# Kernel optimization log

Measured on AMD Instinct MI355X. Metric: run time of the kernel, lower is better.

Reference implementation:

```python
import jax, jax.numpy as jnp
import numpy as np

DIM = 64      # fixed by fuse=BasicConv2d(64,64)
HEADS = 8
B, H, W = 16, 128, 128
CPH = DIM // HEADS  # 8 channels per head


def conv2d(x, w, groups=1, pad=1):
    # x: [B,C,H,W], w: [O, C//groups, kh, kw]
    return jax.lax.conv_general_dilated(
        x, w, window_strides=(1, 1), padding=[(pad, pad), (pad, pad)],
        dimension_numbers=("NCHW", "OIHW", "NCHW"), feature_group_count=groups)


def setup_inputs() -> dict:
    key = jax.random.key(0)
    ks = jax.random.split(key, 8)
    y = jax.random.normal(ks[0], (B, DIM, H, W), jnp.float32)
    # conv3d kernels collapse to their middle depth slice (depth-1 input, zero pad)
    w_qkv = jax.random.normal(ks[1], (3 * DIM, DIM), jnp.float32) * 0.05        # 1x1x1 qkv
    w_dw = jax.random.normal(ks[2], (3 * DIM, 1, 3, 3), jnp.float32) * 0.1      # depthwise 3x3
    w_proj = jax.random.normal(ks[3], (DIM, DIM), jnp.float32) * 0.05           # 1x1x1 project_out
    w_fc = jax.random.normal(ks[4], (9, 3 * HEADS), jnp.float32) * 0.1          # fc: 24->9
    b_fc = jnp.zeros((9,), jnp.float32)
    w_dep = jax.random.normal(ks[5], (DIM, 9, 3, 3), jnp.float32) * 0.1         # grouped: 72->64, groups=8
    b_dep = jnp.zeros((DIM,), jnp.float32)
    temperature = jnp.ones((HEADS, 1, 1), jnp.float32)
    w_fuse = jax.random.normal(ks[6], (DIM, DIM, 3, 3), jnp.float32) * 0.05     # fuse conv, no bias
    bn_gamma = jnp.ones((DIM,), jnp.float32)
    bn_beta = jnp.zeros((DIM,), jnp.float32)
    bn_mean = jnp.zeros((DIM,), jnp.float32)
    bn_var = jnp.ones((DIM,), jnp.float32)
    return dict(y=y, w_qkv=w_qkv, w_dw=w_dw, w_proj=w_proj, w_fc=w_fc, b_fc=b_fc,
                w_dep=w_dep, b_dep=b_dep, temperature=temperature, w_fuse=w_fuse,
                bn_gamma=bn_gamma, bn_beta=bn_beta, bn_mean=bn_mean, bn_var=bn_var)


def reference(y, w_qkv, w_dw, w_proj, w_fc, b_fc, w_dep, b_dep, temperature,
              w_fuse, bn_gamma, bn_beta, bn_mean, bn_var):
    b, c, h, w = y.shape
    # qkv 1x1 conv then 3x3 depthwise conv (groups = 3*DIM)
    qkv = jnp.einsum('oc,bchw->bohw', w_qkv, y)                 # [b,192,h,w]
    qkv = conv2d(qkv, w_dw, groups=3 * DIM, pad=1)
    # dynamic kernel generation branch: flat reshape (row-major, matches torch)
    f_all = qkv.reshape(b, h * w, 3 * HEADS, CPH).transpose(0, 2, 1, 3)  # [b,24,hw,8]
    f_all = jnp.einsum('oc,bcne->bone', w_fc, f_all) + b_fc[None, :, None, None]  # [b,9,hw,8]
    f_conv = f_all.transpose(0, 3, 1, 2).reshape(b, 9 * CPH, h, w)       # [b,72,h,w]
    out_conv = conv2d(f_conv, w_dep, groups=CPH, pad=1) + b_dep[None, :, None, None]
    # channel (transposed) attention with L2-normalize + temperature + softmax
    q, k, v = jnp.split(qkv, 3, axis=1)
    def to_heads(t):
        return t.reshape(b, HEADS, CPH, h * w)
    q, k, v = to_heads(q), to_heads(k), to_heads(v)
    q = q / jnp.maximum(jnp.linalg.norm(q, axis=-1, keepdims=True), 1e-12)
    k = k / jnp.maximum(jnp.linalg.norm(k, axis=-1, keepdims=True), 1e-12)
    attn = jnp.einsum('bhcn,bhdn->bhcd', q, k) * temperature[None]       # [b,8,8,8]
    attn = jax.nn.softmax(attn, axis=-1)
    out = jnp.einsum('bhcd,bhdn->bhcn', attn, v).reshape(b, DIM, h, w)
    out = jnp.einsum('oc,bchw->bohw', w_proj, out)
    output = out + out_conv
    # fuse: conv3x3 (no bias) + BatchNorm (inference stats), then residual + ReLU
    fused = conv2d(output, w_fuse, pad=1)
    scale = (bn_gamma / jnp.sqrt(bn_var + 1e-5))[None, :, None, None]
    fused = (fused - bn_mean[None, :, None, None]) * scale + bn_beta[None, :, None, None]
    return jax.nn.relu(fused + y)
```

## Files before the change

### kernel.cpp

```cpp
#include <hip/hip_runtime.h>
#include <hip/hip_bf16.h>

#define BN 16
#define CC 64
#define HH 128
#define WW 128
#define HW 16384
#define C3 192
#define NHEADS 8


__global__ __launch_bounds__(256) void k_qkv1(const float* __restrict__ y,
                                              const float* __restrict__ w_qkv,
                                              float* __restrict__ out, int chunk) {
    __shared__ float ws[64 * 64];
    int tid = threadIdx.x;
    for (int i = tid; i < 4096; i += 256) {
        int c = i >> 6, o = i & 63;
        ws[i] = w_qkv[(chunk * 64 + o) * 64 + c];
    }
    __syncthreads();
    int bid = blockIdx.x;
    int b = bid >> 6;
    int ptile = bid & 63;
    int pxg = tid & 127;
    int osub = tid >> 7;
    int p0 = ptile * 256 + pxg * 2;
    const float* yb = y + (size_t)b * CC * HW + p0;
    float acc0[32];
    float acc1[32];
#pragma unroll
    for (int o = 0; o < 32; ++o) { acc0[o] = 0.f; acc1[o] = 0.f; }
    for (int c = 0; c < 64; ++c) {
        float2 yv = *(const float2*)(yb + (size_t)c * HW);
        const float* wr = &ws[c * 64 + osub * 32];
#pragma unroll
        for (int o = 0; o < 32; ++o) {
            float w = wr[o];
            acc0[o] = fmaf(w, yv.x, acc0[o]);
            acc1[o] = fmaf(w, yv.y, acc1[o]);
        }
    }
    float* ob = out + (size_t)b * 64 * HW + (size_t)(osub * 32) * HW + p0;
#pragma unroll
    for (int o = 0; o < 32; ++o) {
        *(float2*)(ob + (size_t)o * HW) = make_float2(acc0[o], acc1[o]);
    }
}

__global__ __launch_bounds__(256) void k_dw(const float* __restrict__ in,
                                            const float* __restrict__ w_dw,
                                            float* __restrict__ out, int chunk) {
    int bid = blockIdx.x;
    int tid = threadIdx.x;
    int b = bid >> 11;
    int rem = bid & 2047;
    int ch = rem >> 5;
    int tile = rem & 31;
    int pp = tile * 512 + tid * 2;
    int py = pp >> 7, px = pp & 127;
    const float* ib = in + ((size_t)b * 64 + ch) * HW;
    const float* wr = w_dw + (chunk * 64 + ch) * 9;
    float w[9];
#pragma unroll
    for (int i = 0; i < 9; ++i) w[i] = wr[i];
    float a0 = 0.f, a1 = 0.f;
#pragma unroll
    for (int ky = 0; ky < 3; ++ky) {
        int yy = py + ky - 1;
        bool yok = (unsigned)yy < 128u;
#pragma unroll
        for (int kx = 0; kx < 4; ++kx) {
            int xx = px + kx - 1;
            bool ok = yok && ((unsigned)xx < 128u);
            float v = ok ? ib[yy * 128 + xx] : 0.f;
            if (kx < 3) a0 = fmaf(w[ky * 3 + kx], v, a0);
            if (kx > 0) a1 = fmaf(w[ky * 3 + kx - 1], v, a1);
        }
    }
    *(float2*)(out + ((size_t)b * C3 + chunk * 64 + ch) * HW + pp) = make_float2(a0, a1);
}

__global__ __launch_bounds__(256) void k_fc(const float* __restrict__ qkv,
                                            const float* __restrict__ w_fc,
                                            const float* __restrict__ b_fc,
                                            float* __restrict__ fconv) {
    __shared__ float wf[216];
    __shared__ float bf[9];
    __shared__ float sx[32 * 193];
    int tid = threadIdx.x;
    if (tid < 216) wf[tid] = w_fc[tid];
    if (tid < 9) bf[tid] = b_fc[tid];
    int bid = blockIdx.x;
    int b = bid >> 9;
    int n0 = (bid & 511) * 32;
    const float* src = qkv + (size_t)b * C3 * HW + (size_t)n0 * 192;
    for (int f4 = tid; f4 < 1536; f4 += 256) {
        int f = f4 * 4;
        int nl = f / 192;
        int r = f - nl * 192;
        float4 v = *(const float4*)(src + f);
        float* d = &sx[nl * 193 + r];
        d[0] = v.x; d[1] = v.y; d[2] = v.z; d[3] = v.w;
    }
    __syncthreads();
    int e = tid >> 5, n = tid & 31;
    const float* xr = &sx[n * 193 + e];
    float acc[9];
#pragma unroll
    for (int o = 0; o < 9; ++o) acc[o] = bf[o];
#pragma unroll
    for (int g = 0; g < 24; ++g) {
        float xv = xr[g * 8];
#pragma unroll
        for (int o = 0; o < 9; ++o) acc[o] = fmaf(wf[o * 24 + g], xv, acc[o]);
    }
    float* ob = fconv + (size_t)b * 72 * HW + n0 + n;
#pragma unroll
    for (int o = 0; o < 9; ++o) ob[(size_t)(e * 9 + o) * HW] = acc[o];
}

#define GST 20
__global__ __launch_bounds__(256) void k_gconv(const float* __restrict__ fconv,
                                               const float* __restrict__ w_dep,
                                               const float* __restrict__ b_dep,
                                               float* __restrict__ outO) {
    __shared__ __align__(16) float sm_in[9 * 18 * GST];
    __shared__ __align__(16) float sm_w[81 * 8];
    __shared__ float sm_b[8];
    int tid = threadIdx.x;
    int bid = blockIdx.x;
    int b = bid >> 9;
    int rem = bid & 511;
    int grp = rem >> 6;
    int tile = rem & 63;
    int ty0 = (tile >> 3) * 16, tx0 = (tile & 7) * 16;
    const float* ibase = fconv + ((size_t)b * 72 + grp * 9) * HW;
    for (int i = tid; i < 9 * 324; i += 256) {
        int c = i / 324;
        int r2 = i - c * 324;
        int r = r2 / 18;
        int q = r2 - r * 18;
        int yy = ty0 + r - 1, xx = tx0 + q - 1;
        sm_in[c * (18 * GST) + r * GST + q] =
            ((unsigned)yy < 128u && (unsigned)xx < 128u)
                ? ibase[(size_t)c * HW + yy * 128 + xx] : 0.f;
    }
    for (int i = tid; i < 648; i += 256) {
        int o = i & 7;
        int ik = i >> 3;
        sm_w[i] = w_dep[(size_t)(grp * 8 + o) * 81 + ik];
    }
    if (tid < 8) sm_b[tid] = b_dep[grp * 8 + tid];
    __syncthreads();
    int row = tid >> 4, col = tid & 15;
    float acc[8];
#pragma unroll
    for (int o = 0; o < 8; ++o) acc[o] = sm_b[o];
#pragma unroll
    for (int ic = 0; ic < 9; ++ic) {
        float nb[3][3];
        const float* sc = &sm_in[ic * (18 * GST) + row * GST + col];
#pragma unroll
        for (int r = 0; r < 3; ++r)
#pragma unroll
            for (int q = 0; q < 3; ++q) nb[r][q] = sc[r * GST + q];
        const float* wp = &sm_w[ic * 72];
#pragma unroll
        for (int k = 0; k < 9; ++k) {
            float4 w0 = *(const float4*)(wp + k * 8);
            float4 w1 = *(const float4*)(wp + k * 8 + 4);
            float v = nb[k / 3][k % 3];
            acc[0] = fmaf(w0.x, v, acc[0]);
            acc[1] = fmaf(w0.y, v, acc[1]);
            acc[2] = fmaf(w0.z, v, acc[2]);
            acc[3] = fmaf(w0.w, v, acc[3]);
            acc[4] = fmaf(w1.x, v, acc[4]);
            acc[5] = fmaf(w1.y, v, acc[5]);
            acc[6] = fmaf(w1.z, v, acc[6]);
            acc[7] = fmaf(w1.w, v, acc[7]);
        }
    }
    float* ob = outO + ((size_t)b * 64 + grp * 8) * HW + (ty0 + row) * 128 + tx0 + col;
#pragma unroll
    for (int o = 0; o < 8; ++o) ob[(size_t)o * HW] = acc[o];
}

__global__ __launch_bounds__(256) void k_attn_p(const float* __restrict__ qkv,
                                                float* __restrict__ partial) {
    __shared__ float red[4][64];
    __shared__ float redq[4][8];
    __shared__ float redk[4][8];
    int bid = blockIdx.x;
    int b = bid >> 5, h = (bid >> 2) & 7, seg = bid & 3;
    int tid = threadIdx.x;
    const float* Q = qkv + ((size_t)b * C3 + h * 8) * HW;
    const float* K = Q + (size_t)64 * HW;
    float acc[64], qs[8], ks[8];
#pragma unroll
    for (int j = 0; j < 64; ++j) acc[j] = 0.f;
#pragma unroll
    for (int d = 0; d < 8; ++d) { qs[d] = 0.f; ks[d] = 0.f; }
    int iend = (seg + 1) * 4096;
    for (int i = seg * 4096 + tid; i < iend; i += 256) {
        float qv[8], kv[8];
#pragma unroll
        for (int d = 0; d < 8; ++d) {
            qv[d] = Q[(size_t)d * HW + i];
            kv[d] = K[(size_t)d * HW + i];
        }
#pragma unroll
        for (int d = 0; d < 8; ++d) {
            qs[d] = fmaf(qv[d], qv[d], qs[d]);
            ks[d] = fmaf(kv[d], kv[d], ks[d]);
        }
#pragma unroll
        for (int c = 0; c < 8; ++c)
#pragma unroll
            for (int d = 0; d < 8; ++d)
                acc[c * 8 + d] = fmaf(qv[c], kv[d], acc[c * 8 + d]);
    }
#pragma unroll
    for (int j = 0; j < 64; ++j) {
#pragma unroll
        for (int off = 32; off; off >>= 1) acc[j] += __shfl_down(acc[j], off, 64);
    }
#pragma unroll
    for (int d = 0; d < 8; ++d) {
#pragma unroll
        for (int off = 32; off; off >>= 1) {
            qs[d] += __shfl_down(qs[d], off, 64);
            ks[d] += __shfl_down(ks[d], off, 64);
        }
    }
    int lane = tid & 63, wv = tid >> 6;
    if (lane == 0) {
#pragma unroll
        for (int j = 0; j < 64; ++j) red[wv][j] = acc[j];
#pragma unroll
        for (int d = 0; d < 8; ++d) { redq[wv][d] = qs[d]; redk[wv][d] = ks[d]; }
    }
    __syncthreads();
    float* outp = partial + (size_t)bid * 80;
    if (tid < 64) {
        outp[tid] = red[0][tid] + red[1][tid] + red[2][tid] + red[3][tid];
    } else if (tid < 72) {
        int d = tid - 64;
        outp[64 + d] = redq[0][d] + redq[1][d] + redq[2][d] + redq[3][d];
    } else if (tid < 80) {
        int d = tid - 72;
        outp[72 + d] = redk[0][d] + redk[1][d] + redk[2][d] + redk[3][d];
    }
}

__global__ __launch_bounds__(256) void k_attn_f(const float* __restrict__ partial,
                                                const float* __restrict__ temperature,
                                                float* __restrict__ attn) {
    __shared__ float sm[80];
    __shared__ float lg[64];
    int bh = blockIdx.x;
    int h = bh & 7;
    int tid = threadIdx.x;
    if (tid < 80) {
        const float* pp = partial + (size_t)bh * 4 * 80 + tid;
        sm[tid] = pp[0] + pp[80] + pp[160] + pp[240];
    }
    __syncthreads();
    if (tid < 64) {
        int c = tid >> 3, d = tid & 7;
        float invq = 1.f / fmaxf(sqrtf(sm[64 + c]), 1e-12f);
        float invk = 1.f / fmaxf(sqrtf(sm[72 + d]), 1e-12f);
        lg[tid] = sm[tid] * invq * invk * temperature[h];
    }
    __syncthreads();
    if (tid < 8) {
        int c = tid;
        float m = lg[c * 8];
#pragma unroll
        for (int d = 1; d < 8; ++d) m = fmaxf(m, lg[c * 8 + d]);
        float ssum = 0.f, ex[8];
#pragma unroll
        for (int d = 0; d < 8; ++d) { ex[d] = expf(lg[c * 8 + d] - m); ssum += ex[d]; }
        float inv = 1.f / ssum;
#pragma unroll
        for (int d = 0; d < 8; ++d)
            attn[(size_t)bh * 64 + c * 8 + d] = ex[d] * inv;
    }
}

__global__ __launch_bounds__(256) void k_av_proj(const float* __restrict__ qkv,
                                                 const float* __restrict__ attn,
                                                 const float* __restrict__ w_proj,
                                                 float* __restrict__ outO) {
    __shared__ float at[512];
    __shared__ float wp[4096];
    int tid = threadIdx.x;
    int bid = blockIdx.x;
    int b = bid >> 6, tile = bid & 63;
    for (int i = tid; i < 512; i += 256) at[i] = attn[b * 512 + i];
    for (int i = tid; i < 4096; i += 256) {
        int c = i >> 6, o = i & 63;
        wp[i] = w_proj[o * 64 + c];
    }
    __syncthreads();
    int p = tile * 256 + tid;
    const float* vb = qkv + ((size_t)b * C3 + 128) * HW + p;
    float av[64];
#pragma unroll
    for (int h = 0; h < 8; ++h) {
        float vv[8];
#pragma unroll
        for (int d = 0; d < 8; ++d) vv[d] = vb[(size_t)(h * 8 + d) * HW];
#pragma unroll
        for (int ci = 0; ci < 8; ++ci) {
            float s = 0.f;
#pragma unroll
            for (int d = 0; d < 8; ++d) s = fmaf(at[(h * 8 + ci) * 8 + d], vv[d], s);
            av[h * 8 + ci] = s;
        }
    }
    float* ob = outO + (size_t)b * 64 * HW + p;
    float acc[64];
#pragma unroll
    for (int o = 0; o < 64; ++o) acc[o] = ob[(size_t)o * HW];
    for (int c = 0; c < 64; ++c) {
        float a = av[c];
        const float* wr = &wp[c * 64];
#pragma unroll
        for (int o = 0; o < 64; ++o) acc[o] = fmaf(wr[o], a, acc[o]);
    }
#pragma unroll
    for (int o = 0; o < 64; ++o) ob[(size_t)o * HW] = acc[o];
}

#define ST 20
__global__ __launch_bounds__(256) void k_fuse(const float* __restrict__ outO,
                                              const float* __restrict__ w_fuse,
                                              const float* __restrict__ bn_gamma,
                                              const float* __restrict__ bn_beta,
                                              const float* __restrict__ bn_mean,
                                              const float* __restrict__ bn_var,
                                              const float* __restrict__ y,
                                              float* __restrict__ dout) {
    __shared__ __align__(16) float sm_in[8 * 18 * ST];
    __shared__ __align__(16) float sm_w[8 * 9 * 32];
    __shared__ float sm_sc[64];
    __shared__ float sm_sb[64];
    int tid = threadIdx.x;
    int bid = blockIdx.x;
    int b = bid >> 7;
    int rem = bid & 127;
    int ob32 = rem >> 6;
    int tile = rem & 63;
    int ty0 = (tile >> 3) * 16, tx0 = (tile & 7) * 16;

    if (tid < 64) {
        float sc = bn_gamma[tid] * rsqrtf(bn_var[tid] + 1e-5f);
        sm_sc[tid] = sc;
        sm_sb[tid] = bn_beta[tid] - bn_mean[tid] * sc;
    }

    int osub = tid >> 6;
    int o0 = osub * 8;
    int lane = tid & 63;
    int col = lane & 15;
    int rowg = lane >> 4;
    int r0 = rowg * 4;

    const float* ib = outO + (size_t)b * 64 * HW;
    float acc[4][8];
#pragma unroll
    for (int p = 0; p < 4; ++p)
#pragma unroll
        for (int o = 0; o < 8; ++o) acc[p][o] = 0.f;

    for (int ch = 0; ch < 8; ++ch) {
        int c0 = ch * 8;
        __syncthreads();
        for (int i = tid; i < 8 * 18 * 18; i += 256) {
            int c = i / 324;
            int rem2 = i - c * 324;
            int r = rem2 / 18;
            int q = rem2 - r * 18;
            int yy = ty0 + r - 1;
            int xx = tx0 + q - 1;
            float v = ((unsigned)yy < 128u && (unsigned)xx < 128u)
                          ? ib[(size_t)(c0 + c) * HW + yy * 128 + xx] : 0.f;
            sm_in[c * (18 * ST) + r * ST + q] = v;
        }
        for (int i = tid; i < 8 * 9 * 32; i += 256) {
            int o = i & 31;
            int kk = (i >> 5) % 9;
            int c = i / 288;
            sm_w[(c * 9 + kk) * 32 + o] =
                w_fuse[((size_t)(ob32 * 32 + o) * 64 + (c0 + c)) * 9 + kk];
        }
        __syncthreads();
        for (int cc = 0; cc < 8; ++cc) {
            float nb[6][3];
            const float* sin_c = &sm_in[cc * (18 * ST)];
#pragma unroll
            for (int r = 0; r < 6; ++r)
#pragma unroll
                for (int q = 0; q < 3; ++q)
                    nb[r][q] = sin_c[(r0 + r) * ST + col + q];
            const float* wc = &sm_w[cc * 288 + o0];
#pragma unroll
            for (int k = 0; k < 9; ++k) {
                int ky = k / 3, kx = k % 3;
                float4 w0 = *(const float4*)(wc + k * 32);
                float4 w1 = *(const float4*)(wc + k * 32 + 4);
#pragma unroll
                for (int p = 0; p < 4; ++p) {
                    float v = nb[p + ky][kx];
                    acc[p][0] = fmaf(w0.x, v, acc[p][0]);
                    acc[p][1] = fmaf(w0.y, v, acc[p][1]);
                    acc[p][2] = fmaf(w0.z, v, acc[p][2]);
                    acc[p][3] = fmaf(w0.w, v, acc[p][3]);
                    acc[p][4] = fmaf(w1.x, v, acc[p][4]);
                    acc[p][5] = fmaf(w1.y, v, acc[p][5]);
                    acc[p][6] = fmaf(w1.z, v, acc[p][6]);
                    acc[p][7] = fmaf(w1.w, v, acc[p][7]);
                }
            }
        }
    }
#pragma unroll
    for (int o = 0; o < 8; ++o) {
        int og = ob32 * 32 + o0 + o;
        float sc = sm_sc[og], sb = sm_sb[og];
#pragma unroll
        for (int p = 0; p < 4; ++p) {
            int pyy = ty0 + r0 + p;
            int pxx = tx0 + col;
            size_t idx = ((size_t)b * 64 + og) * HW + pyy * 128 + pxx;
            float v = acc[p][o] * sc + sb + y[idx];
            dout[idx] = fmaxf(v, 0.f);
        }
    }
}

extern "C" void kernel_launch(void* const* d_in, const int* in_sizes, int n_in,
                              void* d_out, int out_size, void* d_ws, size_t ws_size,
                              hipStream_t stream) {
    const float* y           = (const float*)d_in[0];
    const float* w_qkv       = (const float*)d_in[1];
    const float* w_dw        = (const float*)d_in[2];
    const float* w_proj      = (const float*)d_in[3];
    const float* w_fc        = (const float*)d_in[4];
    const float* b_fc        = (const float*)d_in[5];
    const float* w_dep       = (const float*)d_in[6];
    const float* b_dep       = (const float*)d_in[7];
    const float* temperature = (const float*)d_in[8];
    const float* w_fuse      = (const float*)d_in[9];
    const float* bn_gamma    = (const float*)d_in[10];
    const float* bn_beta     = (const float*)d_in[11];
    const float* bn_mean     = (const float*)d_in[12];
    const float* bn_var      = (const float*)d_in[13];
    float* out = (float*)d_out;

    float* ws    = (float*)d_ws;
    float* qkvB  = ws;
    float* bufT  = ws + 25165824;
    float* bufO  = ws + 34603008;
    float* attn  = ws + 42992640;
    float* attnP = ws + 42996736;
    (void)in_sizes; (void)n_in; (void)out_size; (void)ws_size;

    for (int g = 0; g < 2; ++g) {
        const float* yg = y + (size_t)g * 8 * CC * HW;
        float* outg = out + (size_t)g * 8 * CC * HW;
        for (int chunk = 0; chunk < 3; ++chunk) {
            k_qkv1<<<512, 256, 0, stream>>>(yg, w_qkv, bufT, chunk);
            k_dw<<<16384, 256, 0, stream>>>(bufT, w_dw, qkvB, chunk);
        }
        k_fc<<<4096, 256, 0, stream>>>(qkvB, w_fc, b_fc, bufT);
        k_gconv<<<4096, 256, 0, stream>>>(bufT, w_dep, b_dep, bufO);
        k_attn_p<<<256, 256, 0, stream>>>(qkvB, attnP);
        k_attn_f<<<64, 256, 0, stream>>>(attnP, temperature, attn);
        k_av_proj<<<512, 256, 0, stream>>>(qkvB, attn, w_proj, bufO);
        k_fuse<<<1024, 256, 0, stream>>>(bufO, w_fuse, bn_gamma, bn_beta,
                                         bn_mean, bn_var, yg, outg);
    }
}
```

Measured before the change: 1.025 ms.

## Fuse qkv 1x1 conv with depthwise 3x3 conv using halo tiles in shared memory

Replaces the separate qkv pointwise conv and depthwise conv kernels (launched per 64-channel chunk) with one kernel. Each block computes 16 output channels for a 16x16 spatial tile plus a 1-pixel halo in shared memory, then applies the depthwise 3x3 directly from shared memory. This removes the intermediate buffer write and read and cuts six launches down to one per group. In exchange, halo pixels are recomputed and y is re-read once for each of the 12 output-channel groups.

```diff
diff --git a/kernel.cpp b/kernel.cpp
--- a/kernel.cpp
+++ b/kernel.cpp
@@ -10,75 +10,87 @@
 #define NHEADS 8
 
 
-__global__ __launch_bounds__(256) void k_qkv1(const float* __restrict__ y,
-                                              const float* __restrict__ w_qkv,
-                                              float* __restrict__ out, int chunk) {
-    __shared__ float ws[64 * 64];
-    int tid = threadIdx.x;
-    for (int i = tid; i < 4096; i += 256) {
-        int c = i >> 6, o = i & 63;
-        ws[i] = w_qkv[(chunk * 64 + o) * 64 + c];
-    }
-    __syncthreads();
-    int bid = blockIdx.x;
-    int b = bid >> 6;
-    int ptile = bid & 63;
-    int pxg = tid & 127;
-    int osub = tid >> 7;
-    int p0 = ptile * 256 + pxg * 2;
-    const float* yb = y + (size_t)b * CC * HW + p0;
-    float acc0[32];
-    float acc1[32];
-#pragma unroll
-    for (int o = 0; o < 32; ++o) { acc0[o] = 0.f; acc1[o] = 0.f; }
-    for (int c = 0; c < 64; ++c) {
-        float2 yv = *(const float2*)(yb + (size_t)c * HW);
-        const float* wr = &ws[c * 64 + osub * 32];
-#pragma unroll
-        for (int o = 0; o < 32; ++o) {
-            float w = wr[o];
-            acc0[o] = fmaf(w, yv.x, acc0[o]);
-            acc1[o] = fmaf(w, yv.y, acc1[o]);
-        }
-    }
-    float* ob = out + (size_t)b * 64 * HW + (size_t)(osub * 32) * HW + p0;
-#pragma unroll
-    for (int o = 0; o < 32; ++o) {
-        *(float2*)(ob + (size_t)o * HW) = make_float2(acc0[o], acc1[o]);
-    }
-}
-
-__global__ __launch_bounds__(256) void k_dw(const float* __restrict__ in,
-                                            const float* __restrict__ w_dw,
-                                            float* __restrict__ out, int chunk) {
-    int bid = blockIdx.x;
-    int tid = threadIdx.x;
-    int b = bid >> 11;
-    int rem = bid & 2047;
-    int ch = rem >> 5;
-    int tile = rem & 31;
-    int pp = tile * 512 + tid * 2;
-    int py = pp >> 7, px = pp & 127;
-    const float* ib = in + ((size_t)b * 64 + ch) * HW;
-    const float* wr = w_dw + (chunk * 64 + ch) * 9;
-    float w[9];
-#pragma unroll
-    for (int i = 0; i < 9; ++i) w[i] = wr[i];
-    float a0 = 0.f, a1 = 0.f;
-#pragma unroll
-    for (int ky = 0; ky < 3; ++ky) {
-        int yy = py + ky - 1;
-        bool yok = (unsigned)yy < 128u;
-#pragma unroll
-        for (int kx = 0; kx < 4; ++kx) {
-            int xx = px + kx - 1;
-            bool ok = yok && ((unsigned)xx < 128u);
-            float v = ok ? ib[yy * 128 + xx] : 0.f;
-            if (kx < 3) a0 = fmaf(w[ky * 3 + kx], v, a0);
-            if (kx > 0) a1 = fmaf(w[ky * 3 + kx - 1], v, a1);
-        }
-    }
-    *(float2*)(out + ((size_t)b * C3 + chunk * 64 + ch) * HW + pp) = make_float2(a0, a1);
+__global__ __launch_bounds__(256) void k_qkvdw2(const float* __restrict__ y,
+                                                const float* __restrict__ w_qkv,
+                                                const float* __restrict__ w_dw,
+                                                float* __restrict__ qkvB) {
+    __shared__ __align__(16) float sm_w1[64 * 16];
+    __shared__ __align__(16) float sm_y[8 * 324];
+    __shared__ __align__(16) float sm_q[16 * 328];
+    __shared__ float sm_wd[16 * 9];
+    int tid = threadIdx.x;
+    int bid = blockIdx.x;
+    int b = bid / 768;
+    int rem = bid - b * 768;
+    int tile = rem / 12;
+    int oc16 = rem - tile * 12;
+    int ty0 = (tile >> 3) * 16, tx0 = (tile & 7) * 16;
+
+    for (int i = tid; i < 1024; i += 256) {
+        int c = i >> 4, o = i & 15;
+        sm_w1[i] = w_qkv[(size_t)(oc16 * 16 + o) * 64 + c];
+    }
+    if (tid < 144) sm_wd[tid] = w_dw[(size_t)oc16 * 144 + tid];
+
+    const float* yb = y + (size_t)b * CC * HW;
+    float acc0[16], acc1[16];
+#pragma unroll
+    for (int o = 0; o < 16; ++o) { acc0[o] = 0.f; acc1[o] = 0.f; }
+    bool p2 = tid < 68;
+
+    for (int c8 = 0; c8 < 8; ++c8) {
+        __syncthreads();
+        for (int i = tid; i < 2592; i += 256) {
+            int c = i / 324;
+            int p = i - c * 324;
+            int r = p / 18, q = p - r * 18;
+            int yy = ty0 + r - 1, xx = tx0 + q - 1;
+            sm_y[i] = ((unsigned)yy < 128u && (unsigned)xx < 128u)
+                          ? yb[(size_t)(c8 * 8 + c) * HW + yy * 128 + xx] : 0.f;
+        }
+        __syncthreads();
+#pragma unroll
+        for (int cc = 0; cc < 8; ++cc) {
+            float yv0 = sm_y[cc * 324 + tid];
+            float yv1 = p2 ? sm_y[cc * 324 + 256 + tid] : 0.f;
+            const float* wr = &sm_w1[(c8 * 8 + cc) * 16];
+#pragma unroll
+            for (int o4 = 0; o4 < 4; ++o4) {
+                float4 w = *(const float4*)(wr + o4 * 4);
+                acc0[o4 * 4 + 0] = fmaf(w.x, yv0, acc0[o4 * 4 + 0]);
+                acc0[o4 * 4 + 1] = fmaf(w.y, yv0, acc0[o4 * 4 + 1]);
+                acc0[o4 * 4 + 2] = fmaf(w.z, yv0, acc0[o4 * 4 + 2]);
+                acc0[o4 * 4 + 3] = fmaf(w.w, yv0, acc0[o4 * 4 + 3]);
+                acc1[o4 * 4 + 0] = fmaf(w.x, yv1, acc1[o4 * 4 + 0]);
+                acc1[o4 * 4 + 1] = fmaf(w.y, yv1, acc1[o4 * 4 + 1]);
+                acc1[o4 * 4 + 2] = fmaf(w.z, yv1, acc1[o4 * 4 + 2]);
+                acc1[o4 * 4 + 3] = fmaf(w.w, yv1, acc1[o4 * 4 + 3]);
+            }
+        }
+    }
+#pragma unroll
+    for (int o = 0; o < 16; ++o) {
+        sm_q[o * 328 + tid] = acc0[o];
+        if (p2) sm_q[o * 328 + 256 + tid] = acc1[o];
+    }
+    __syncthreads();
+    int ch = tid >> 4, col = tid & 15;
+    float wd[9];
+#pragma unroll
+    for (int k = 0; k < 9; ++k) wd[k] = sm_wd[ch * 9 + k];
+    const float* sq = &sm_q[ch * 328 + col];
+    float* ob = qkvB + ((size_t)b * C3 + oc16 * 16 + ch) * HW
+                + (size_t)ty0 * 128 + tx0 + col;
+    for (int row = 0; row < 16; ++row) {
+        const float* sr = sq + row * 18;
+        float a = 0.f;
+#pragma unroll
+        for (int ky = 0; ky < 3; ++ky)
+#pragma unroll
+            for (int kx = 0; kx < 3; ++kx)
+                a = fmaf(wd[ky * 3 + kx], sr[ky * 18 + kx], a);
+        ob[row * 128] = a;
+    }
 }
 
 __global__ __launch_bounds__(256) void k_fc(const float* __restrict__ qkv,
@@ -470,10 +482,7 @@
     for (int g = 0; g < 2; ++g) {
         const float* yg = y + (size_t)g * 8 * CC * HW;
         float* outg = out + (size_t)g * 8 * CC * HW;
-        for (int chunk = 0; chunk < 3; ++chunk) {
-            k_qkv1<<<512, 256, 0, stream>>>(yg, w_qkv, bufT, chunk);
-            k_dw<<<16384, 256, 0, stream>>>(bufT, w_dw, qkvB, chunk);
-        }
+        k_qkvdw2<<<6144, 256, 0, stream>>>(yg, w_qkv, w_dw, qkvB);
         k_fc<<<4096, 256, 0, stream>>>(qkvB, w_fc, b_fc, bufT);
         k_gconv<<<4096, 256, 0, stream>>>(bufT, w_dep, b_dep, bufO);
         k_attn_p<<<256, 256, 0, stream>>>(qkvB, attnP);
```

Result: slower. 1.802 ms (+75.8%).
